# Optimization experiments

Hardware: AMD Instinct MI355X
Metric: run time of the kernel (lower is better)

## Reference

```python
import jax, jax.numpy as jnp
import numpy as np

N = 50000
E = 800000
IN_CH = 512
OUT_CH = 64
ITERATIONS = 3  # adjacency power order; iterations-1 spmm steps


def setup_inputs() -> dict:
    key = jax.random.key(0)
    k1, k2, k3, k4, k5 = jax.random.split(key, 5)
    adj_indices = jax.random.randint(k1, (2, E), 0, N, dtype=jnp.int32)
    adj_values = jax.random.uniform(k2, (E,), dtype=jnp.float32)
    features = jax.random.normal(k3, (N, IN_CH), dtype=jnp.float32)
    # xavier-uniform init bounds
    bw = float(np.sqrt(6.0 / (IN_CH + OUT_CH)))
    weight = jax.random.uniform(k4, (IN_CH, OUT_CH), minval=-bw, maxval=bw, dtype=jnp.float32)
    bb = float(np.sqrt(6.0 / (1 + OUT_CH)))
    bias = jax.random.uniform(k5, (1, OUT_CH), minval=-bb, maxval=bb, dtype=jnp.float32)
    return {"adj_indices": adj_indices, "adj_values": adj_values,
            "features": features, "weight": weight, "bias": bias}


def reference(adj_indices, adj_values, features, weight, bias):
    # dense projection: [N, in] @ [in, out] -> [N, out]
    x = features @ weight
    # dropout is identity in eval mode (training=False)
    row, col = adj_indices[0], adj_indices[1]
    # (iterations - 1) sparse-dense matmuls: x <- A @ x
    for _ in range(ITERATIONS - 1):
        gathered = adj_values[:, None] * x[col]          # [E, out]
        x = jax.ops.segment_sum(gathered, row, num_segments=N)
    return x + bias
```

## Files before the change

### kernel.cpp

```cpp
#include <hip/hip_runtime.h>
#include <hip/hip_bf16.h>
#include <hip/hip_fp16.h>

#define NN 50000
#define INCH 512
#define OUTCH 64
#define NTILES 3125
#define MAXD 96
#define GB 782
#define SB 256

typedef __attribute__((ext_vector_type(8))) short short8;
typedef __attribute__((ext_vector_type(4))) float floatx4;

__device__ __forceinline__ unsigned packbf2(float a, float b) {
    __hip_bfloat162 h = __float22bfloat162_rn(make_float2(a, b));
    unsigned r;
    __builtin_memcpy(&r, &h, 4);
    return r;
}
__device__ __forceinline__ unsigned short f2bf(float f) {
    unsigned u = __float_as_uint(f);
    return (unsigned short)((u + 0x7FFFu + ((u >> 16) & 1u)) >> 16);
}
__device__ __forceinline__ float bf2f(unsigned short u) {
    return __uint_as_float(((unsigned)u) << 16);
}

__global__ __launch_bounds__(256) void prep_kernel(const float* __restrict__ W,
                                                   unsigned short* __restrict__ Wbf,
                                                   int* __restrict__ deg) {
    const int i = blockIdx.x * 256 + threadIdx.x;
    if (i < NN) deg[i] = 0;
    if (i < INCH * OUTCH) {
        const int k = i >> 6;
        const int n = i & 63;
        Wbf[n * INCH + k] = f2bf(W[i]);
    }
}

__global__ __launch_bounds__(256, 4) void fused_gemm_scatter(
        const float* __restrict__ A, const unsigned short* __restrict__ Wbf,
        unsigned short* __restrict__ C,
        const int* __restrict__ rows, const int* __restrict__ cols,
        const float* __restrict__ vals, int* __restrict__ deg,
        unsigned* __restrict__ ell, int E_) {
    __shared__ unsigned short ldsT[4][16 * 64];
    const int t = threadIdx.x;

    if (blockIdx.x >= GB) {
        for (int e = (blockIdx.x - GB) * 256 + t; e < E_; e += SB * 256) {
            const int r = rows[e];
            const int slot = atomicAdd(&deg[r], 1);
            const unsigned short hv = __half_as_ushort(__float2half(vals[e]));
            if (slot < MAXD)
                ell[(size_t)r * MAXD + slot] = (unsigned)cols[e] | ((unsigned)hv << 16);
        }
        return;
    }

    const int lane = t & 63;
    const int wave = t >> 6;
    const int tile = blockIdx.x * 4 + wave;
    if (tile >= NTILES) return;
    const int rbase = tile * 16;
    const int frow = lane & 15;
    const int quad = lane >> 4;
    const float* Ap = A + (size_t)(rbase + frow) * INCH + quad * 8;
    const unsigned short* Bp = Wbf + frow * INCH + quad * 8;

    floatx4 acc[4] = {floatx4{0,0,0,0}, floatx4{0,0,0,0}, floatx4{0,0,0,0}, floatx4{0,0,0,0}};

#pragma unroll
    for (int c = 0; c < 16; ++c) {
        const float4 a0 = *(const float4*)(Ap + c * 32);
        const float4 a1 = *(const float4*)(Ap + c * 32 + 4);
        short8 bfr[4];
#pragma unroll
        for (int f = 0; f < 4; ++f)
            bfr[f] = *(const short8*)(Bp + (size_t)f * 16 * INCH + c * 32);
        uint4 au;
        au.x = packbf2(a0.x, a0.y);
        au.y = packbf2(a0.z, a0.w);
        au.z = packbf2(a1.x, a1.y);
        au.w = packbf2(a1.z, a1.w);
        const short8 af = *(const short8*)&au;
#pragma unroll
        for (int f = 0; f < 4; ++f)
            acc[f] = __builtin_amdgcn_mfma_f32_16x16x32_bf16(af, bfr[f], acc[f], 0, 0, 0);
    }

    unsigned short* myT = ldsT[wave];
#pragma unroll
    for (int f = 0; f < 4; ++f)
#pragma unroll
        for (int reg = 0; reg < 4; ++reg)
            myT[(quad * 4 + reg) * 64 + f * 16 + frow] = f2bf(acc[f][reg]);
    unsigned short* Cw = C + (size_t)rbase * OUTCH;
#pragma unroll
    for (int it = 0; it < 2; ++it) {
        const short8 v = *(const short8*)&myT[it * 512 + lane * 8];
        *(short8*)(Cw + it * 512 + lane * 8) = v;
    }
}

template <bool LAST>
__global__ __launch_bounds__(256) void spmm_ell(const int* __restrict__ deg,
                                                const unsigned* __restrict__ ell,
                                                const unsigned short* __restrict__ xin,
                                                void* __restrict__ xout_,
                                                const float* __restrict__ bias) {
    const int t = threadIdx.x;
    const int lane = t & 63;
    const int eslot = lane >> 4;
    const int c4 = (lane & 15) * 4;
    const int row = blockIdx.x * 4 + (t >> 6);
    const int d = deg[row];
    const unsigned* ebase = ell + (size_t)row * MAXD;
    float4 acc = make_float4(0.f, 0.f, 0.f, 0.f);
    for (int i = eslot; i < d; i += 4) {
        const unsigned p = ebase[i];
        const ushort4 xv = *(const ushort4*)(xin + (size_t)(p & 0xFFFFu) * OUTCH + c4);
        const float v = __half2float(__ushort_as_half((unsigned short)(p >> 16)));
        acc.x = fmaf(v, bf2f(xv.x), acc.x);
        acc.y = fmaf(v, bf2f(xv.y), acc.y);
        acc.z = fmaf(v, bf2f(xv.z), acc.z);
        acc.w = fmaf(v, bf2f(xv.w), acc.w);
    }
    acc.x += __shfl_xor(acc.x, 16, 64); acc.y += __shfl_xor(acc.y, 16, 64);
    acc.z += __shfl_xor(acc.z, 16, 64); acc.w += __shfl_xor(acc.w, 16, 64);
    acc.x += __shfl_xor(acc.x, 32, 64); acc.y += __shfl_xor(acc.y, 32, 64);
    acc.z += __shfl_xor(acc.z, 32, 64); acc.w += __shfl_xor(acc.w, 32, 64);
    if (eslot == 0) {
        if (LAST) {
            const float4 bv = *(const float4*)(bias + c4);
            acc.x += bv.x; acc.y += bv.y; acc.z += bv.z; acc.w += bv.w;
            *(float4*)((float*)xout_ + (size_t)row * OUTCH + c4) = acc;
        } else {
            ushort4 o;
            o.x = f2bf(acc.x); o.y = f2bf(acc.y); o.z = f2bf(acc.z); o.w = f2bf(acc.w);
            *(ushort4*)((unsigned short*)xout_ + (size_t)row * OUTCH + c4) = o;
        }
    }
}

extern "C" void kernel_launch(void* const* d_in, const int* in_sizes, int n_in,
                              void* d_out, int out_size, void* d_ws, size_t ws_size,
                              hipStream_t stream) {
    const int*   adj   = (const int*)d_in[0];
    const float* avals = (const float*)d_in[1];
    const float* feat  = (const float*)d_in[2];
    const float* W     = (const float*)d_in[3];
    const float* bias  = (const float*)d_in[4];
    float* out = (float*)d_out;

    const int E_ = in_sizes[1];
    const int* rows = adj;
    const int* cols = adj + E_;

    unsigned short* x0  = (unsigned short*)d_ws;
    unsigned short* x1  = x0 + (size_t)NN * OUTCH;
    unsigned short* Wbf = x1 + (size_t)NN * OUTCH;
    unsigned* ell = (unsigned*)(Wbf + (size_t)OUTCH * INCH);
    int* deg = (int*)(ell + (size_t)NN * MAXD);

    prep_kernel<<<(NN + 255) / 256, 256, 0, stream>>>(W, Wbf, deg);

    fused_gemm_scatter<<<GB + SB, 256, 0, stream>>>(feat, Wbf, x0, rows, cols, avals,
                                                    deg, ell, E_);

    spmm_ell<false><<<NN / 4, 256, 0, stream>>>(deg, ell, x0, x1, nullptr);
    spmm_ell<true><<<NN / 4, 256, 0, stream>>>(deg, ell, x1, out, bias);
}
```

Before: 260.7 us.

## Stage bf16 weights in swizzled LDS, batch A loads, prefetch ELL indices

Each GEMM block copies the full bf16 weight matrix into LDS with an XOR swizzle and reads B fragments from LDS instead of global memory. A-row loads are grouped into two batches of eight chunks to raise outstanding memory requests. Out-of-range waves stay alive for the barrier and only skip the store. The SpMM loop prefetches the next packed ELL entry one iteration ahead. The 64KB of LDS per block lowers achievable occupancy, which may hurt latency hiding for the bandwidth-bound feature stream.

```diff
diff --git a/kernel.cpp b/kernel.cpp
--- a/kernel.cpp
+++ b/kernel.cpp
@@ -39,12 +39,13 @@
     }
 }
 
-__global__ __launch_bounds__(256, 4) void fused_gemm_scatter(
+__global__ __launch_bounds__(256) void fused_gemm_scatter(
         const float* __restrict__ A, const unsigned short* __restrict__ Wbf,
         unsigned short* __restrict__ C,
         const int* __restrict__ rows, const int* __restrict__ cols,
         const float* __restrict__ vals, int* __restrict__ deg,
         unsigned* __restrict__ ell, int E_) {
+    __shared__ unsigned short Ws[64 * 512];
     __shared__ unsigned short ldsT[4][16 * 64];
     const int t = threadIdx.x;
 
@@ -59,48 +60,72 @@
         return;
     }
 
+    {
+        const int n = t & 63;
+        const int gset = t >> 6;
+#pragma unroll
+        for (int i = 0; i < 16; ++i) {
+            const int g = gset * 16 + i;
+            const short8 v = *(const short8*)(Wbf + n * INCH + g * 8);
+            const int pg = g ^ (n & 7);
+            *(short8*)&Ws[n * 512 + pg * 8] = v;
+        }
+    }
+    __syncthreads();
+
     const int lane = t & 63;
     const int wave = t >> 6;
-    const int tile = blockIdx.x * 4 + wave;
-    if (tile >= NTILES) return;
+    const int tileRaw = blockIdx.x * 4 + wave;
+    const int tile = (tileRaw < NTILES) ? tileRaw : (NTILES - 1);
+    const bool active = (tileRaw < NTILES);
     const int rbase = tile * 16;
     const int frow = lane & 15;
     const int quad = lane >> 4;
     const float* Ap = A + (size_t)(rbase + frow) * INCH + quad * 8;
-    const unsigned short* Bp = Wbf + frow * INCH + quad * 8;
+    const int fsw = frow & 7;
 
     floatx4 acc[4] = {floatx4{0,0,0,0}, floatx4{0,0,0,0}, floatx4{0,0,0,0}, floatx4{0,0,0,0}};
 
-#pragma unroll
-    for (int c = 0; c < 16; ++c) {
-        const float4 a0 = *(const float4*)(Ap + c * 32);
-        const float4 a1 = *(const float4*)(Ap + c * 32 + 4);
-        short8 bfr[4];
+    float4 abuf[16];
+    for (int h = 0; h < 2; ++h) {
+#pragma unroll
+        for (int c = 0; c < 8; ++c) {
+            abuf[c * 2 + 0] = *(const float4*)(Ap + (h * 8 + c) * 32);
+            abuf[c * 2 + 1] = *(const float4*)(Ap + (h * 8 + c) * 32 + 4);
+        }
+#pragma unroll
+        for (int c = 0; c < 8; ++c) {
+            const int cc = h * 8 + c;
+            const float4 a0 = abuf[c * 2 + 0];
+            const float4 a1 = abuf[c * 2 + 1];
+            uint4 au;
+            au.x = packbf2(a0.x, a0.y);
+            au.y = packbf2(a0.z, a0.w);
+            au.z = packbf2(a1.x, a1.y);
+            au.w = packbf2(a1.z, a1.w);
+            const short8 af = *(const short8*)&au;
+            const int pg = (cc * 4 + quad) ^ fsw;
+#pragma unroll
+            for (int f = 0; f < 4; ++f) {
+                const short8 bfr = *(const short8*)&Ws[(f * 16 + frow) * 512 + pg * 8];
+                acc[f] = __builtin_amdgcn_mfma_f32_16x16x32_bf16(af, bfr, acc[f], 0, 0, 0);
+            }
+        }
+    }
+
+    if (active) {
+        unsigned short* myT = ldsT[wave];
 #pragma unroll
         for (int f = 0; f < 4; ++f)
-            bfr[f] = *(const short8*)(Bp + (size_t)f * 16 * INCH + c * 32);
-        uint4 au;
-        au.x = packbf2(a0.x, a0.y);
-        au.y = packbf2(a0.z, a0.w);
-        au.z = packbf2(a1.x, a1.y);
-        au.w = packbf2(a1.z, a1.w);
-        const short8 af = *(const short8*)&au;
-#pragma unroll
-        for (int f = 0; f < 4; ++f)
-            acc[f] = __builtin_amdgcn_mfma_f32_16x16x32_bf16(af, bfr[f], acc[f], 0, 0, 0);
-    }
-
-    unsigned short* myT = ldsT[wave];
-#pragma unroll
-    for (int f = 0; f < 4; ++f)
-#pragma unroll
-        for (int reg = 0; reg < 4; ++reg)
-            myT[(quad * 4 + reg) * 64 + f * 16 + frow] = f2bf(acc[f][reg]);
-    unsigned short* Cw = C + (size_t)rbase * OUTCH;
-#pragma unroll
-    for (int it = 0; it < 2; ++it) {
-        const short8 v = *(const short8*)&myT[it * 512 + lane * 8];
-        *(short8*)(Cw + it * 512 + lane * 8) = v;
+#pragma unroll
+            for (int reg = 0; reg < 4; ++reg)
+                myT[(quad * 4 + reg) * 64 + f * 16 + frow] = f2bf(acc[f][reg]);
+        unsigned short* Cw = C + (size_t)rbase * OUTCH;
+#pragma unroll
+        for (int it = 0; it < 2; ++it) {
+            const short8 v = *(const short8*)&myT[it * 512 + lane * 8];
+            *(short8*)(Cw + it * 512 + lane * 8) = v;
+        }
     }
 }
 
@@ -118,14 +143,19 @@
     const int d = deg[row];
     const unsigned* ebase = ell + (size_t)row * MAXD;
     float4 acc = make_float4(0.f, 0.f, 0.f, 0.f);
-    for (int i = eslot; i < d; i += 4) {
-        const unsigned p = ebase[i];
+    int i = eslot;
+    unsigned p = (i < d) ? ebase[i] : 0u;
+    while (i < d) {
+        const int inext = i + 4;
+        const unsigned pn = (inext < d) ? ebase[inext] : 0u;
         const ushort4 xv = *(const ushort4*)(xin + (size_t)(p & 0xFFFFu) * OUTCH + c4);
         const float v = __half2float(__ushort_as_half((unsigned short)(p >> 16)));
         acc.x = fmaf(v, bf2f(xv.x), acc.x);
         acc.y = fmaf(v, bf2f(xv.y), acc.y);
         acc.z = fmaf(v, bf2f(xv.z), acc.z);
         acc.w = fmaf(v, bf2f(xv.w), acc.w);
+        p = pn;
+        i = inext;
     }
     acc.x += __shfl_xor(acc.x, 16, 64); acc.y += __shfl_xor(acc.y, 16, 64);
     acc.z += __shfl_xor(acc.z, 16, 64); acc.w += __shfl_xor(acc.w, 16, 64);
```

Result: slower. 271.6 us (+4.2%).

## Process 32-row GEMM tiles per wave, reorder scatter blocks, prefetch ELL entries

Applied to the files above, without the earlier changes.

Each wave now computes two 16-row tiles so every W fragment it loads feeds both, halving W reloads per output row, and the feature matrix is read with nontemporal loads. Scatter blocks are moved to the front of the grid so the ELL build is scheduled first, alongside the GEMM. The SpMM loop software-prefetches the next ELL entry to hide the index-load latency. Costs are higher register pressure, fewer GEMM waves for parallelism, and clamped duplicate work on the tail tile.

```diff
diff --git a/kernel.cpp b/kernel.cpp
--- a/kernel.cpp
+++ b/kernel.cpp
@@ -5,10 +5,10 @@
 #define NN 50000
 #define INCH 512
 #define OUTCH 64
-#define NTILES 3125
 #define MAXD 96
-#define GB 782
 #define SB 256
+#define NT32 1563
+#define GB2 391
 
 typedef __attribute__((ext_vector_type(8))) short short8;
 typedef __attribute__((ext_vector_type(4))) float floatx4;
@@ -48,8 +48,8 @@
     __shared__ unsigned short ldsT[4][16 * 64];
     const int t = threadIdx.x;
 
-    if (blockIdx.x >= GB) {
-        for (int e = (blockIdx.x - GB) * 256 + t; e < E_; e += SB * 256) {
+    if (blockIdx.x < SB) {
+        for (int e = blockIdx.x * 256 + t; e < E_; e += SB * 256) {
             const int r = rows[e];
             const int slot = atomicAdd(&deg[r], 1);
             const unsigned short hv = __half_as_ushort(__float2half(vals[e]));
@@ -61,46 +61,62 @@
 
     const int lane = t & 63;
     const int wave = t >> 6;
-    const int tile = blockIdx.x * 4 + wave;
-    if (tile >= NTILES) return;
-    const int rbase = tile * 16;
+    const int tileRaw = (blockIdx.x - SB) * 4 + wave;
+    const int tile = (tileRaw < NT32) ? tileRaw : (NT32 - 1);
+    const int rbase = tile * 32;
     const int frow = lane & 15;
     const int quad = lane >> 4;
-    const float* Ap = A + (size_t)(rbase + frow) * INCH + quad * 8;
+
+    int r0 = rbase + frow;       if (r0 > NN - 1) r0 = NN - 1;
+    int r1 = rbase + 16 + frow;  if (r1 > NN - 1) r1 = NN - 1;
+    const float* Ap0 = A + (size_t)r0 * INCH + quad * 8;
+    const float* Ap1 = A + (size_t)r1 * INCH + quad * 8;
     const unsigned short* Bp = Wbf + frow * INCH + quad * 8;
 
-    floatx4 acc[4] = {floatx4{0,0,0,0}, floatx4{0,0,0,0}, floatx4{0,0,0,0}, floatx4{0,0,0,0}};
+    floatx4 acc0[4] = {floatx4{0,0,0,0}, floatx4{0,0,0,0}, floatx4{0,0,0,0}, floatx4{0,0,0,0}};
+    floatx4 acc1[4] = {floatx4{0,0,0,0}, floatx4{0,0,0,0}, floatx4{0,0,0,0}, floatx4{0,0,0,0}};
 
 #pragma unroll
     for (int c = 0; c < 16; ++c) {
-        const float4 a0 = *(const float4*)(Ap + c * 32);
-        const float4 a1 = *(const float4*)(Ap + c * 32 + 4);
+        const floatx4 a00 = __builtin_nontemporal_load((const floatx4*)(Ap0 + c * 32));
+        const floatx4 a01 = __builtin_nontemporal_load((const floatx4*)(Ap0 + c * 32 + 4));
+        const floatx4 a10 = __builtin_nontemporal_load((const floatx4*)(Ap1 + c * 32));
+        const floatx4 a11 = __builtin_nontemporal_load((const floatx4*)(Ap1 + c * 32 + 4));
         short8 bfr[4];
 #pragma unroll
         for (int f = 0; f < 4; ++f)
             bfr[f] = *(const short8*)(Bp + (size_t)f * 16 * INCH + c * 32);
-        uint4 au;
-        au.x = packbf2(a0.x, a0.y);
-        au.y = packbf2(a0.z, a0.w);
-        au.z = packbf2(a1.x, a1.y);
-        au.w = packbf2(a1.z, a1.w);
-        const short8 af = *(const short8*)&au;
+        uint4 u0, u1;
+        u0.x = packbf2(a00[0], a00[1]); u0.y = packbf2(a00[2], a00[3]);
+        u0.z = packbf2(a01[0], a01[1]); u0.w = packbf2(a01[2], a01[3]);
+        u1.x = packbf2(a10[0], a10[1]); u1.y = packbf2(a10[2], a10[3]);
+        u1.z = packbf2(a11[0], a11[1]); u1.w = packbf2(a11[2], a11[3]);
+        const short8 af0 = *(const short8*)&u0;
+        const short8 af1 = *(const short8*)&u1;
 #pragma unroll
-        for (int f = 0; f < 4; ++f)
-            acc[f] = __builtin_amdgcn_mfma_f32_16x16x32_bf16(af, bfr[f], acc[f], 0, 0, 0);
+        for (int f = 0; f < 4; ++f) {
+            acc0[f] = __builtin_amdgcn_mfma_f32_16x16x32_bf16(af0, bfr[f], acc0[f], 0, 0, 0);
+            acc1[f] = __builtin_amdgcn_mfma_f32_16x16x32_bf16(af1, bfr[f], acc1[f], 0, 0, 0);
+        }
     }
 
     unsigned short* myT = ldsT[wave];
 #pragma unroll
-    for (int f = 0; f < 4; ++f)
+    for (int s = 0; s < 2; ++s) {
+        const floatx4* acc = s ? acc1 : acc0;
 #pragma unroll
-        for (int reg = 0; reg < 4; ++reg)
-            myT[(quad * 4 + reg) * 64 + f * 16 + frow] = f2bf(acc[f][reg]);
-    unsigned short* Cw = C + (size_t)rbase * OUTCH;
+        for (int f = 0; f < 4; ++f)
 #pragma unroll
-    for (int it = 0; it < 2; ++it) {
-        const short8 v = *(const short8*)&myT[it * 512 + lane * 8];
-        *(short8*)(Cw + it * 512 + lane * 8) = v;
+            for (int reg = 0; reg < 4; ++reg)
+                myT[(quad * 4 + reg) * 64 + f * 16 + frow] = f2bf(acc[f][reg]);
+        unsigned short* Cw = C + (size_t)(rbase + s * 16) * OUTCH;
+#pragma unroll
+        for (int it = 0; it < 2; ++it) {
+            const int rowg = rbase + s * 16 + it * 8 + (lane >> 3);
+            const short8 v = *(const short8*)&myT[it * 512 + lane * 8];
+            if (rowg < NN)
+                *(short8*)(Cw + it * 512 + lane * 8) = v;
+        }
     }
 }
 
@@ -118,14 +134,19 @@
     const int d = deg[row];
     const unsigned* ebase = ell + (size_t)row * MAXD;
     float4 acc = make_float4(0.f, 0.f, 0.f, 0.f);
-    for (int i = eslot; i < d; i += 4) {
-        const unsigned p = ebase[i];
+    int i = eslot;
+    unsigned p = (i < d) ? ebase[i] : 0u;
+    while (i < d) {
+        const int inext = i + 4;
+        const unsigned pn = (inext < d) ? ebase[inext] : 0u;
         const ushort4 xv = *(const ushort4*)(xin + (size_t)(p & 0xFFFFu) * OUTCH + c4);
         const float v = __half2float(__ushort_as_half((unsigned short)(p >> 16)));
         acc.x = fmaf(v, bf2f(xv.x), acc.x);
         acc.y = fmaf(v, bf2f(xv.y), acc.y);
         acc.z = fmaf(v, bf2f(xv.z), acc.z);
         acc.w = fmaf(v, bf2f(xv.w), acc.w);
+        p = pn;
+        i = inext;
     }
     acc.x += __shfl_xor(acc.x, 16, 64); acc.y += __shfl_xor(acc.y, 16, 64);
     acc.z += __shfl_xor(acc.z, 16, 64); acc.w += __shfl_xor(acc.w, 16, 64);
@@ -166,8 +187,8 @@
 
     prep_kernel<<<(NN + 255) / 256, 256, 0, stream>>>(W, Wbf, deg);
 
-    fused_gemm_scatter<<<GB + SB, 256, 0, stream>>>(feat, Wbf, x0, rows, cols, avals,
-                                                    deg, ell, E_);
+    fused_gemm_scatter<<<SB + GB2, 256, 0, stream>>>(feat, Wbf, x0, rows, cols, avals,
+                                                     deg, ell, E_);
 
     spmm_ell<false><<<NN / 4, 256, 0, stream>>>(deg, ell, x0, x1, nullptr);
     spmm_ell<true><<<NN / 4, 256, 0, stream>>>(deg, ell, x1, out, bias);
```

New measurement: 262.4 us. Within noise of the previous version (+0.7%).
